# Performance work log

Measured on AMD Instinct MI355X. Metric: run time of the kernel, lower is better.

The kernel has to match this reference:

```python
import jax, jax.numpy as jnp
import numpy as np

E = 32      # num_experts
K = 4       # num_experts_per_tok
C = 1280


def setup_inputs() -> dict:
    key = jax.random.key(0)
    k0, k1, k2, k3, k4 = jax.random.split(key, 5)
    B, S, D, I = 4, 2048, 1024, 512
    return {
        "hidden_states": jax.random.normal(k0, (B, S, D), jnp.float32),
        "router_w": jax.random.normal(k1, (E, D), jnp.float32) * 0.02,   # nn.Linear(hidden, E).weight
        "gate_w": jax.random.normal(k2, (E, I, D), jnp.float32) * 0.02,
        "up_w": jax.random.normal(k3, (E, I, D), jnp.float32) * 0.02,
        "down_w": jax.random.normal(k4, (E, D, I), jnp.float32) * 0.02,
    }


def reference(hidden_states, router_w, gate_w, up_w, down_w):
    B, S, D = hidden_states.shape
    x = hidden_states.reshape(-1, D)                       # [T, D]
    T = x.shape[0]

    # Router: softmax in fp32, top-k, renormalize (norm_topk_prob=True)
    router_logits = x @ router_w.T                          # [T, E]
    probs = jax.nn.softmax(router_logits.astype(jnp.float32), axis=-1)
    w, sel = jax.lax.top_k(probs, K)                        # [T, K]
    w = w / jnp.sum(w, axis=-1, keepdims=True)
    w = w.astype(x.dtype)

    # Flatten (token, slot) dispatch rows
    e_flat = sel.reshape(-1)                                # [T*K]
    tok = jnp.repeat(jnp.arange(T), K)                      # [T*K]

    # Position of each row within its expert's buffer
    oh = jax.nn.one_hot(e_flat, E, dtype=jnp.int32)         # [T*K, E]
    pos = jnp.take_along_axis(jnp.cumsum(oh, axis=0), e_flat[:, None], axis=1)[:, 0] - 1
    valid = pos < C

    # Dispatch: scatter tokens into [E, C, D]; overflow rows go to slot C and are dropped
    pos_w = jnp.minimum(pos, C)
    buf = jnp.zeros((E, C + 1, D), x.dtype).at[e_flat, pos_w].set(x[tok])[:, :C]

    # Per-expert SwiGLU MLP as grouped matmuls
    g = jnp.einsum('ecd,eid->eci', buf, gate_w)
    u = jnp.einsum('ecd,eid->eci', buf, up_w)
    h = jax.nn.silu(g) * u
    y = jnp.einsum('eci,edi->ecd', h, down_w)               # [E, C, D]

    # Combine: gather expert outputs back and scatter-add into tokens
    pos_r = jnp.minimum(pos, C - 1)
    gathered = y[e_flat, pos_r]                             # [T*K, D]
    coef = w.reshape(-1) * valid.astype(x.dtype)
    final = jax.ops.segment_sum(gathered * coef[:, None], tok, num_segments=T)

    return final.reshape(B, S, D), router_logits
```

## Files before the change

### kernel.cpp

```cpp
#include <hip/hip_runtime.h>

#define T_TOK 8192
#define D_DIM 1024
#define E_NUM 32
#define K_TOP 4
#define CAP 1280
#define I_DIM 512

typedef float f32x4 __attribute__((ext_vector_type(4)));
typedef short s16x8 __attribute__((ext_vector_type(8)));

static __device__ __forceinline__ unsigned short f2bf(float f) {
    unsigned int u = __float_as_uint(f);
    unsigned int r = (u + 0x7fffu + ((u >> 16) & 1u)) >> 16;
    return (unsigned short)r;
}
static __device__ __forceinline__ float bf2f(unsigned short s) {
    return __uint_as_float(((unsigned int)s) << 16);
}

static __device__ __forceinline__ void gload16(const unsigned short* g, unsigned short* l) {
    __builtin_amdgcn_global_load_lds(
        (const __attribute__((address_space(1))) unsigned int*)g,
        (__attribute__((address_space(3))) unsigned int*)l,
        16, 0, 0);
}

#define GW_F4 4194304L
__global__ __launch_bounds__(256) void cvt_kernel(
    const float* __restrict__ gw,
    const float* __restrict__ uw, const float* __restrict__ dw,
    unsigned short* __restrict__ gbf,
    unsigned short* __restrict__ ubf, unsigned short* __restrict__ dbf) {
    long i = (long)blockIdx.x * 256 + threadIdx.x;
    const float* src; unsigned short* dst; long off;
    if (i < GW_F4)        { src = gw; dst = gbf; off = i; }
    else if (i < 2*GW_F4) { src = uw; dst = ubf; off = i - GW_F4; }
    else                  { src = dw; dst = dbf; off = i - 2*GW_F4; }
    float4 v = ((const float4*)src)[off];
    ushort4 b;
    b.x = f2bf(v.x); b.y = f2bf(v.y); b.z = f2bf(v.z); b.w = f2bf(v.w);
    ((ushort4*)dst)[off] = b;
}

__global__ __launch_bounds__(256) void router_kernel(
    const float* __restrict__ x, const float* __restrict__ rw,
    float* __restrict__ logits, unsigned short* __restrict__ xbf) {
    int t = (blockIdx.x * 256 + threadIdx.x) >> 6;
    int lane = threadIdx.x & 63;
    const float* xr = x + (size_t)t * D_DIM;
    float xf[16];
#pragma unroll
    for (int j = 0; j < 16; ++j) xf[j] = xr[lane + 64 * j];
    unsigned short* xb = xbf + (size_t)t * D_DIM;
#pragma unroll
    for (int j = 0; j < 16; ++j) xb[lane + 64 * j] = f2bf(xf[j]);
#pragma unroll 1
    for (int e = 0; e < E_NUM; ++e) {
        const float* wr = rw + (size_t)e * D_DIM;
        float acc = 0.f;
#pragma unroll
        for (int j = 0; j < 16; ++j) acc = fmaf(xf[j], wr[lane + 64 * j], acc);
#pragma unroll
        for (int off = 32; off; off >>= 1) acc += __shfl_xor(acc, off);
        if (lane == 0) logits[(size_t)t * E_NUM + e] = acc;
    }
}

__global__ __launch_bounds__(256) void topk_kernel(
    const float* __restrict__ logits,
    int* __restrict__ counts, int* __restrict__ rowtok,
    int* __restrict__ tokslot, float* __restrict__ tokcoef) {
    __shared__ float lg[256 * 33];
    __shared__ int hist[E_NUM];
    __shared__ int base[E_NUM];
    int tid = threadIdx.x;
    int t0 = blockIdx.x * 256;
    if (tid < E_NUM) hist[tid] = 0;
#pragma unroll
    for (int i = 0; i < E_NUM; ++i) {
        int idx = i * 256 + tid;
        lg[(idx >> 5) * 33 + (idx & 31)] = logits[(size_t)t0 * E_NUM + idx];
    }
    __syncthreads();

    float p[E_NUM];
    float m = -1e30f;
#pragma unroll
    for (int e = 0; e < E_NUM; ++e) { p[e] = lg[tid * 33 + e]; m = fmaxf(m, p[e]); }
#pragma unroll
    for (int e = 0; e < E_NUM; ++e) p[e] = __expf(p[e] - m);

    float wv[K_TOP]; int sel[K_TOP];
#pragma unroll
    for (int k = 0; k < K_TOP; ++k) {
        float best = -1.0f; int bi = 0;
#pragma unroll
        for (int e = 0; e < E_NUM; ++e) if (p[e] > best) { best = p[e]; bi = e; }
        wv[k] = best; sel[k] = bi; p[bi] = -2.0f;
    }

    int lofs[K_TOP];
#pragma unroll
    for (int k = 0; k < K_TOP; ++k) lofs[k] = atomicAdd(&hist[sel[k]], 1);
    __syncthreads();
    if (tid < E_NUM) base[tid] = atomicAdd(&counts[tid], hist[tid]);
    __syncthreads();

    float inv = 1.0f / (wv[0] + wv[1] + wv[2] + wv[3]);
    int t = t0 + tid;
#pragma unroll
    for (int k = 0; k < K_TOP; ++k) {
        int e = sel[k];
        int slot = base[e] + lofs[k];
        if (slot < CAP) {
            rowtok[e * CAP + slot] = t;
            tokslot[t * K_TOP + k] = e * CAP + slot;
        } else {
            tokslot[t * K_TOP + k] = -1;
        }
        tokcoef[t * K_TOP + k] = wv[k] * inv;
    }
}

__global__ __launch_bounds__(512, 2) void gateup_kernel(
    const unsigned short* __restrict__ xbf,
    const unsigned short* __restrict__ gbf, const unsigned short* __restrict__ ubf,
    const int* __restrict__ counts, const int* __restrict__ rowtok,
    unsigned short* __restrict__ h_ws) {
    int bid = blockIdx.x;
    int xcd = bid & 7;
    int slot = bid >> 3;
    int e = xcd + 8 * (slot / 20);
    int r = slot % 20;
    int mt = r >> 2;
    int nt = r & 3;
    int n_e = counts[e]; if (n_e > CAP) n_e = CAP;
    if (mt * 256 >= n_e) return;

    __shared__ unsigned short As[2][256 * 64];
    __shared__ unsigned short Bg[2][128 * 64];
    __shared__ unsigned short Bu[2][128 * 64];
    __shared__ int toks[256];

    int tid = threadIdx.x, lane = tid & 63, wv = tid >> 6;
    if (tid < 256) {
        int rr = mt * 256 + tid;
        toks[tid] = (rr < n_e) ? rowtok[e * CAP + rr] : rowtok[e * CAP];
    }
    __syncthreads();

    int row8 = tid >> 3;
    int c8 = (tid & 7) * 8;
    int ldst = tid * 8;
    const unsigned short* aB[4];
#pragma unroll
    for (int j = 0; j < 4; ++j)
        aB[j] = xbf + (size_t)toks[j * 64 + row8] * D_DIM + c8;
    const unsigned short* gB[2];
    const unsigned short* uB[2];
#pragma unroll
    for (int j = 0; j < 2; ++j) {
        gB[j] = gbf + ((size_t)e * I_DIM + nt * 128 + j * 64 + row8) * D_DIM + c8;
        uB[j] = ubf + ((size_t)e * I_DIM + nt * 128 + j * 64 + row8) * D_DIM + c8;
    }

    int wm = (wv >> 1) * 64;
    int wn = (wv & 1) * 64;
    int fr = lane & 15;
    int fc = (lane >> 4) * 8;

    f32x4 accg[4][4] = {};
    f32x4 accu[4][4] = {};

#pragma unroll
    for (int j = 0; j < 4; ++j) gload16(aB[j], &As[0][j * 4096 + ldst]);
#pragma unroll
    for (int j = 0; j < 2; ++j) {
        gload16(gB[j], &Bg[0][j * 4096 + ldst]);
        gload16(uB[j], &Bu[0][j * 4096 + ldst]);
    }

    for (int kb = 0; kb < D_DIM; kb += 64) {
        int p = (kb >> 6) & 1;
        __syncthreads();

        if (kb + 64 < D_DIM) {
            int q = p ^ 1, k2 = kb + 64;
#pragma unroll
            for (int j = 0; j < 4; ++j) gload16(aB[j] + k2, &As[q][j * 4096 + ldst]);
#pragma unroll
            for (int j = 0; j < 2; ++j) {
                gload16(gB[j] + k2, &Bg[q][j * 4096 + ldst]);
                gload16(uB[j] + k2, &Bu[q][j * 4096 + ldst]);
            }
        }

#pragma unroll
        for (int kk = 0; kk < 2; ++kk) {
            s16x8 af[4], bgf[4], buf_[4];
#pragma unroll
            for (int mi = 0; mi < 4; ++mi)
                af[mi] = *(const s16x8*)&As[p][(wm + mi * 16 + fr) * 64 + kk * 32 + fc];
#pragma unroll
            for (int ni = 0; ni < 4; ++ni) {
                bgf[ni]  = *(const s16x8*)&Bg[p][(wn + ni * 16 + fr) * 64 + kk * 32 + fc];
                buf_[ni] = *(const s16x8*)&Bu[p][(wn + ni * 16 + fr) * 64 + kk * 32 + fc];
            }
#pragma unroll
            for (int mi = 0; mi < 4; ++mi)
#pragma unroll
                for (int ni = 0; ni < 4; ++ni) {
                    accg[mi][ni] = __builtin_amdgcn_mfma_f32_16x16x32_bf16(af[mi], bgf[ni],  accg[mi][ni], 0, 0, 0);
                    accu[mi][ni] = __builtin_amdgcn_mfma_f32_16x16x32_bf16(af[mi], buf_[ni], accu[mi][ni], 0, 0, 0);
                }
        }
    }

    int rq = (lane >> 4) * 4;
    int cq = lane & 15;
#pragma unroll
    for (int mi = 0; mi < 4; ++mi)
#pragma unroll
        for (int ni = 0; ni < 4; ++ni)
#pragma unroll
            for (int rr = 0; rr < 4; ++rr) {
                int grow = mt * 256 + wm + mi * 16 + rq + rr;
                if (grow < n_e) {
                    float g = accg[mi][ni][rr];
                    float hv = g / (1.0f + __expf(-g)) * accu[mi][ni][rr];
                    int icol = nt * 128 + wn + ni * 16 + cq;
                    h_ws[((size_t)e * CAP + grow) * I_DIM + icol] = f2bf(hv);
                }
            }
}

__global__ __launch_bounds__(512, 2) void down_kernel(
    const unsigned short* __restrict__ h_ws, const unsigned short* __restrict__ dbf,
    const int* __restrict__ counts, unsigned short* __restrict__ y_ws) {
    int bid = blockIdx.x;
    int xcd = bid & 7;
    int slot = bid >> 3;
    int e = xcd + 8 * (slot / 20);
    int r = slot % 20;
    int mt = r >> 2;
    int nt = r & 3;
    int n_e = counts[e]; if (n_e > CAP) n_e = CAP;
    if (mt * 256 >= n_e) return;

    __shared__ unsigned short As[2][256 * 64];
    __shared__ unsigned short Bd[2][256 * 64];

    int tid = threadIdx.x, lane = tid & 63, wv = tid >> 6;

    int row8 = tid >> 3;
    int c8 = (tid & 7) * 8;
    int ldst = tid * 8;
    const unsigned short* aB[4];
    const unsigned short* bB[4];
#pragma unroll
    for (int j = 0; j < 4; ++j) {
        aB[j] = h_ws + ((size_t)e * CAP + mt * 256 + j * 64 + row8) * I_DIM + c8;
        bB[j] = dbf  + ((size_t)e * D_DIM + nt * 256 + j * 64 + row8) * I_DIM + c8;
    }

    int wm = (wv >> 2) * 128;
    int wn = (wv & 3) * 64;
    int fr = lane & 15;
    int fc = (lane >> 4) * 8;

    f32x4 acc[8][4] = {};

#pragma unroll
    for (int j = 0; j < 4; ++j) {
        gload16(aB[j], &As[0][j * 4096 + ldst]);
        gload16(bB[j], &Bd[0][j * 4096 + ldst]);
    }

    for (int kb = 0; kb < I_DIM; kb += 64) {
        int p = (kb >> 6) & 1;
        __syncthreads();

        if (kb + 64 < I_DIM) {
            int q = p ^ 1, k2 = kb + 64;
#pragma unroll
            for (int j = 0; j < 4; ++j) {
                gload16(aB[j] + k2, &As[q][j * 4096 + ldst]);
                gload16(bB[j] + k2, &Bd[q][j * 4096 + ldst]);
            }
        }

#pragma unroll
        for (int kk = 0; kk < 2; ++kk) {
            s16x8 af[8], bf[4];
#pragma unroll
            for (int mi = 0; mi < 8; ++mi)
                af[mi] = *(const s16x8*)&As[p][(wm + mi * 16 + fr) * 64 + kk * 32 + fc];
#pragma unroll
            for (int ni = 0; ni < 4; ++ni)
                bf[ni] = *(const s16x8*)&Bd[p][(wn + ni * 16 + fr) * 64 + kk * 32 + fc];
#pragma unroll
            for (int mi = 0; mi < 8; ++mi)
#pragma unroll
                for (int ni = 0; ni < 4; ++ni)
                    acc[mi][ni] = __builtin_amdgcn_mfma_f32_16x16x32_bf16(af[mi], bf[ni], acc[mi][ni], 0, 0, 0);
        }
    }

    int rq = (lane >> 4) * 4;
    int cq = lane & 15;
#pragma unroll
    for (int mi = 0; mi < 8; ++mi)
#pragma unroll
        for (int ni = 0; ni < 4; ++ni)
#pragma unroll
            for (int rr = 0; rr < 4; ++rr) {
                int grow = mt * 256 + wm + mi * 16 + rq + rr;
                if (grow < n_e) {
                    int dcol = nt * 256 + wn + ni * 16 + cq;
                    y_ws[((size_t)e * CAP + grow) * D_DIM + dcol] = f2bf(acc[mi][ni][rr]);
                }
            }
}

__global__ __launch_bounds__(256) void combine_kernel(
    const unsigned short* __restrict__ y_ws,
    const int* __restrict__ tokslot, const float* __restrict__ tokcoef,
    float* __restrict__ out) {
    int t = (blockIdx.x * 256 + threadIdx.x) >> 6;
    int lane = threadIdx.x & 63;
    float acc[16] = {};
#pragma unroll
    for (int k = 0; k < K_TOP; ++k) {
        int slot = tokslot[t * K_TOP + k];
        if (slot >= 0) {
            float c = tokcoef[t * K_TOP + k];
            const unsigned short* row = y_ws + (size_t)slot * D_DIM + lane * 16;
            s16x8 v0 = *(const s16x8*)row;
            s16x8 v1 = *(const s16x8*)(row + 8);
#pragma unroll
            for (int j = 0; j < 8; ++j) acc[j]     = fmaf(c, bf2f((unsigned short)v0[j]), acc[j]);
#pragma unroll
            for (int j = 0; j < 8; ++j) acc[8 + j] = fmaf(c, bf2f((unsigned short)v1[j]), acc[8 + j]);
        }
    }
    float* o = out + (size_t)t * D_DIM + lane * 16;
#pragma unroll
    for (int j = 0; j < 4; ++j)
        ((float4*)o)[j] = make_float4(acc[4 * j], acc[4 * j + 1], acc[4 * j + 2], acc[4 * j + 3]);
}

extern "C" void kernel_launch(void* const* d_in, const int* in_sizes, int n_in,
                              void* d_out, int out_size, void* d_ws, size_t ws_size,
                              hipStream_t stream) {
    const float* x  = (const float*)d_in[0];
    const float* rw = (const float*)d_in[1];
    const float* gw = (const float*)d_in[2];
    const float* uw = (const float*)d_in[3];
    const float* dw = (const float*)d_in[4];
    float* out = (float*)d_out;
    float* logits = out + (size_t)T_TOK * D_DIM;

    char* ws = (char*)d_ws;
    size_t off = 0;
    unsigned short* xbf = (unsigned short*)(ws + off); off += (size_t)T_TOK * D_DIM * 2;
    unsigned short* gbf = (unsigned short*)(ws + off); off += (size_t)E_NUM * I_DIM * D_DIM * 2;
    unsigned short* ubf = (unsigned short*)(ws + off); off += (size_t)E_NUM * I_DIM * D_DIM * 2;
    unsigned short* y_ws = xbf;
    unsigned short* dbf = (unsigned short*)(ws + off); off += (size_t)E_NUM * D_DIM * I_DIM * 2;
    unsigned short* h_ws = (unsigned short*)(ws + off); off += (size_t)E_NUM * CAP * I_DIM * 2;
    int* counts = (int*)(ws + off); off += 256;
    int* rowtok = (int*)(ws + off); off += (size_t)E_NUM * CAP * 4;
    int* tokslot = (int*)(ws + off); off += (size_t)T_TOK * K_TOP * 4;
    float* tokcoef = (float*)(ws + off); off += (size_t)T_TOK * K_TOP * 4;

    hipMemsetAsync(counts, 0, E_NUM * 4, stream);

    cvt_kernel<<<(int)((3 * GW_F4) / 256), 256, 0, stream>>>(gw, uw, dw, gbf, ubf, dbf);
    router_kernel<<<T_TOK / 4, 256, 0, stream>>>(x, rw, logits, xbf);
    topk_kernel<<<T_TOK / 256, 256, 0, stream>>>(logits, counts, rowtok, tokslot, tokcoef);
    gateup_kernel<<<E_NUM * (CAP / 256) * (I_DIM / 128), 512, 0, stream>>>(xbf, gbf, ubf, counts, rowtok, h_ws);
    down_kernel<<<E_NUM * (CAP / 256) * (D_DIM / 256), 512, 0, stream>>>(h_ws, dbf, counts, y_ws);
    combine_kernel<<<T_TOK / 4, 256, 0, stream>>>(y_ws, tokslot, tokcoef, out);
}
```

Baseline: 500.4 us.

## Swizzle LDS tiles and prefetch two stages ahead in expert GEMM kernels

Applies an XOR swizzle to the global-to-LDS column placement and the matching MFMA fragment reads, to remove LDS bank conflicts in both the gate/up and down grouped GEMMs. Replaces the single-stage prefetch loop with a two-stages-ahead schedule that uses explicit vmcnt waits and barriers, so loads for tile k+2 can be in flight while tile k is computed. Raises wave priority around the MFMA block. Correctness depends on the vmcnt(8) count matching exactly the number of outstanding loads per stage, and on the second barrier guarding reuse of each buffer.

```diff
diff --git a/kernel.cpp b/kernel.cpp
--- a/kernel.cpp
+++ b/kernel.cpp
@@ -151,7 +151,7 @@
     __syncthreads();
 
     int row8 = tid >> 3;
-    int c8 = (tid & 7) * 8;
+    int c8 = (((tid & 7) ^ (row8 & 7)) * 8);
     int ldst = tid * 8;
     const unsigned short* aB[4];
 #pragma unroll
@@ -169,43 +169,32 @@
     int wn = (wv & 1) * 64;
     int fr = lane & 15;
     int fc = (lane >> 4) * 8;
+    int fsw = (fr & 7) << 3;
 
     f32x4 accg[4][4] = {};
     f32x4 accu[4][4] = {};
 
-#pragma unroll
-    for (int j = 0; j < 4; ++j) gload16(aB[j], &As[0][j * 4096 + ldst]);
-#pragma unroll
-    for (int j = 0; j < 2; ++j) {
-        gload16(gB[j], &Bg[0][j * 4096 + ldst]);
-        gload16(uB[j], &Bu[0][j * 4096 + ldst]);
-    }
-
-    for (int kb = 0; kb < D_DIM; kb += 64) {
-        int p = (kb >> 6) & 1;
-        __syncthreads();
-
-        if (kb + 64 < D_DIM) {
-            int q = p ^ 1, k2 = kb + 64;
-#pragma unroll
-            for (int j = 0; j < 4; ++j) gload16(aB[j] + k2, &As[q][j * 4096 + ldst]);
-#pragma unroll
-            for (int j = 0; j < 2; ++j) {
-                gload16(gB[j] + k2, &Bg[q][j * 4096 + ldst]);
-                gload16(uB[j] + k2, &Bu[q][j * 4096 + ldst]);
-            }
-        }
-
+    auto stage = [&](int kt) {
+        int q = kt & 1, k2 = kt * 64;
+#pragma unroll
+        for (int j = 0; j < 4; ++j) gload16(aB[j] + k2, &As[q][j * 4096 + ldst]);
+#pragma unroll
+        for (int j = 0; j < 2; ++j) {
+            gload16(gB[j] + k2, &Bg[q][j * 4096 + ldst]);
+            gload16(uB[j] + k2, &Bu[q][j * 4096 + ldst]);
+        }
+    };
+    auto compute = [&](int p) {
 #pragma unroll
         for (int kk = 0; kk < 2; ++kk) {
             s16x8 af[4], bgf[4], buf_[4];
 #pragma unroll
             for (int mi = 0; mi < 4; ++mi)
-                af[mi] = *(const s16x8*)&As[p][(wm + mi * 16 + fr) * 64 + kk * 32 + fc];
+                af[mi] = *(const s16x8*)&As[p][(wm + mi * 16 + fr) * 64 + ((kk * 32 + fc) ^ fsw)];
 #pragma unroll
             for (int ni = 0; ni < 4; ++ni) {
-                bgf[ni]  = *(const s16x8*)&Bg[p][(wn + ni * 16 + fr) * 64 + kk * 32 + fc];
-                buf_[ni] = *(const s16x8*)&Bu[p][(wn + ni * 16 + fr) * 64 + kk * 32 + fc];
+                bgf[ni]  = *(const s16x8*)&Bg[p][(wn + ni * 16 + fr) * 64 + ((kk * 32 + fc) ^ fsw)];
+                buf_[ni] = *(const s16x8*)&Bu[p][(wn + ni * 16 + fr) * 64 + ((kk * 32 + fc) ^ fsw)];
             }
 #pragma unroll
             for (int mi = 0; mi < 4; ++mi)
@@ -215,7 +204,24 @@
                     accu[mi][ni] = __builtin_amdgcn_mfma_f32_16x16x32_bf16(af[mi], buf_[ni], accu[mi][ni], 0, 0, 0);
                 }
         }
-    }
+    };
+
+    stage(0); stage(1);
+    for (int kt = 0; kt < 15; ++kt) {
+        int p = kt & 1;
+        asm volatile("s_waitcnt vmcnt(8)" ::: "memory");
+        asm volatile("s_barrier" ::: "memory");
+        __builtin_amdgcn_s_setprio(1);
+        compute(p);
+        __builtin_amdgcn_s_setprio(0);
+        asm volatile("s_barrier" ::: "memory");
+        if (kt < 14) stage(kt + 2);
+    }
+    asm volatile("s_waitcnt vmcnt(0)" ::: "memory");
+    asm volatile("s_barrier" ::: "memory");
+    __builtin_amdgcn_s_setprio(1);
+    compute(1);
+    __builtin_amdgcn_s_setprio(0);
 
     int rq = (lane >> 4) * 4;
     int cq = lane & 15;
@@ -254,7 +260,7 @@
     int tid = threadIdx.x, lane = tid & 63, wv = tid >> 6;
 
     int row8 = tid >> 3;
-    int c8 = (tid & 7) * 8;
+    int c8 = (((tid & 7) ^ (row8 & 7)) * 8);
     int ldst = tid * 8;
     const unsigned short* aB[4];
     const unsigned short* bB[4];
@@ -268,44 +274,52 @@
     int wn = (wv & 3) * 64;
     int fr = lane & 15;
     int fc = (lane >> 4) * 8;
+    int fsw = (fr & 7) << 3;
 
     f32x4 acc[8][4] = {};
 
-#pragma unroll
-    for (int j = 0; j < 4; ++j) {
-        gload16(aB[j], &As[0][j * 4096 + ldst]);
-        gload16(bB[j], &Bd[0][j * 4096 + ldst]);
-    }
-
-    for (int kb = 0; kb < I_DIM; kb += 64) {
-        int p = (kb >> 6) & 1;
-        __syncthreads();
-
-        if (kb + 64 < I_DIM) {
-            int q = p ^ 1, k2 = kb + 64;
-#pragma unroll
-            for (int j = 0; j < 4; ++j) {
-                gload16(aB[j] + k2, &As[q][j * 4096 + ldst]);
-                gload16(bB[j] + k2, &Bd[q][j * 4096 + ldst]);
-            }
-        }
-
+    auto stage = [&](int kt) {
+        int q = kt & 1, k2 = kt * 64;
+#pragma unroll
+        for (int j = 0; j < 4; ++j) {
+            gload16(aB[j] + k2, &As[q][j * 4096 + ldst]);
+            gload16(bB[j] + k2, &Bd[q][j * 4096 + ldst]);
+        }
+    };
+    auto compute = [&](int p) {
 #pragma unroll
         for (int kk = 0; kk < 2; ++kk) {
             s16x8 af[8], bf[4];
 #pragma unroll
             for (int mi = 0; mi < 8; ++mi)
-                af[mi] = *(const s16x8*)&As[p][(wm + mi * 16 + fr) * 64 + kk * 32 + fc];
+                af[mi] = *(const s16x8*)&As[p][(wm + mi * 16 + fr) * 64 + ((kk * 32 + fc) ^ fsw)];
 #pragma unroll
             for (int ni = 0; ni < 4; ++ni)
-                bf[ni] = *(const s16x8*)&Bd[p][(wn + ni * 16 + fr) * 64 + kk * 32 + fc];
+                bf[ni] = *(const s16x8*)&Bd[p][(wn + ni * 16 + fr) * 64 + ((kk * 32 + fc) ^ fsw)];
 #pragma unroll
             for (int mi = 0; mi < 8; ++mi)
 #pragma unroll
                 for (int ni = 0; ni < 4; ++ni)
                     acc[mi][ni] = __builtin_amdgcn_mfma_f32_16x16x32_bf16(af[mi], bf[ni], acc[mi][ni], 0, 0, 0);
         }
-    }
+    };
+
+    stage(0); stage(1);
+    for (int kt = 0; kt < 7; ++kt) {
+        int p = kt & 1;
+        asm volatile("s_waitcnt vmcnt(8)" ::: "memory");
+        asm volatile("s_barrier" ::: "memory");
+        __builtin_amdgcn_s_setprio(1);
+        compute(p);
+        __builtin_amdgcn_s_setprio(0);
+        asm volatile("s_barrier" ::: "memory");
+        if (kt < 6) stage(kt + 2);
+    }
+    asm volatile("s_waitcnt vmcnt(0)" ::: "memory");
+    asm volatile("s_barrier" ::: "memory");
+    __builtin_amdgcn_s_setprio(1);
+    compute(1);
+    __builtin_amdgcn_s_setprio(0);
 
     int rq = (lane >> 4) * 4;
     int cq = lane & 15;
```

Result: faster. 465.1 us (-7.1%).
